# Kernel tuning notes

Hardware: AMD Instinct MI355X
Metric: run time of the kernel (lower is better)

The kernel has to match this reference:

```python
import jax, jax.numpy as jnp
import numpy as np

V = 100000   # vertices
C = 64       # in channels
D = 64       # out channels
W = 8        # weight matrices
DEG = 16     # neighbors per vertex
E = V * DEG  # edges


def setup_inputs() -> dict:
    key = jax.random.key(0)
    k = jax.random.split(key, 6)
    data = jax.random.normal(k[0], (V, C), dtype=jnp.float32)
    # fixed-degree adjacency: vertex i has DEG neighbors (arbitrary dst)
    edge_src = jnp.repeat(jnp.arange(V, dtype=jnp.int32), DEG)        # [E] sorted
    edge_dst = jax.random.randint(k[1], (E,), 0, V, dtype=jnp.int32)  # [E]
    edge_vals = jnp.full((E,), 1.0 / DEG, dtype=jnp.float32)          # row-normalized
    var_u = 0.1 * jax.random.normal(k[2], (C, W), dtype=jnp.float32)
    var_c = 0.1 * jax.random.normal(k[3], (W,), dtype=jnp.float32)
    var_w = 0.1 * jax.random.normal(k[4], (W, C, D), dtype=jnp.float32)
    var_b = 0.1 * jax.random.normal(k[5], (D,), dtype=jnp.float32)
    return {"data": data, "edge_src": edge_src, "edge_dst": edge_dst,
            "edge_vals": edge_vals, "var_u": var_u, "var_c": var_c,
            "var_w": var_w, "var_b": var_b}


def reference(data, edge_src, edge_dst, edge_vals, var_u, var_c, var_w, var_b):
    # translation_invariant=True => var_v = -var_u
    num_v = data.shape[0]
    x_u = data @ var_u            # [V, W]
    x_v = data @ (-var_u)         # [V, W]
    # edge logits and exp-normalize over the W weight matrices (softmax == exp/sum)
    logits = x_u[edge_src] + x_v[edge_dst] + var_c   # [E, W]
    q = jax.nn.softmax(logits, axis=-1)              # [E, W]
    # gathered neighbor features, pre-scaled by adjacency values
    x_sep = data[edge_dst] * edge_vals[:, None]      # [E, C]
    y = jnp.zeros((num_v, var_w.shape[-1]), dtype=data.dtype)
    for m in range(var_c.shape[0]):  # small fixed loop over W weight matrices
        agg = jax.ops.segment_sum(q[:, m:m + 1] * x_sep, edge_src,
                                  num_segments=num_v)  # [V, C]
        y = y + agg @ var_w[m]                          # [V, D]
    return y + var_b
```

## Files before the change

### kernel.cpp

```cpp
#include <hip/hip_runtime.h>

typedef _Float16 half2_t __attribute__((ext_vector_type(2)));
typedef _Float16 half4_t __attribute__((ext_vector_type(4)));
typedef _Float16 half8_t __attribute__((ext_vector_type(8)));
typedef __attribute__((ext_vector_type(4))) float f32x4;

#define NV 100000
#define NTILE 6250
#define GRID 512
#define LDSZ 81920

#define VMWAIT(N) asm volatile("s_waitcnt vmcnt(" #N ")" ::: "memory")
#define LGKM0     asm volatile("s_waitcnt lgkmcnt(0)" ::: "memory")
#define FENCE     asm volatile("" ::: "memory")

__device__ __forceinline__ unsigned cvt_pk_u(float a, float b) {
  auto h = __builtin_amdgcn_cvt_pkrtz(a, b);
  return __builtin_bit_cast(unsigned, h);
}
__device__ __forceinline__ half2_t u2h(unsigned u) { return __builtin_bit_cast(half2_t, u); }
__device__ __forceinline__ unsigned lds_off(const void* p) {
  return (unsigned)(size_t)(const __attribute__((address_space(3))) char*)p;
}
__device__ __forceinline__ void load16_to_lds(const void* g, void* s) {
  __builtin_amdgcn_global_load_lds(
      (const __attribute__((address_space(1))) unsigned int*)g,
      (__attribute__((address_space(3))) unsigned int*)s, 16, 0, 0);
}

__global__ __launch_bounds__(256) void k1_prep(const float* __restrict__ data,
                                               const float* __restrict__ var_u,
                                               const float* __restrict__ var_w,
                                               unsigned short* __restrict__ data_h,
                                               unsigned short* __restrict__ xu_h,
                                               unsigned short* __restrict__ Bt) {
  __shared__ float u_lds[512];
  int tid = threadIdx.x;
  if (blockIdx.x < 128) {
    int t = blockIdx.x * 256 + tid;
    int d = t >> 9, k = t & 511;
    _Float16 h = (_Float16)var_w[k * 64 + d];
    Bt[t] = __builtin_bit_cast(unsigned short, h);
  }
  u_lds[tid] = var_u[tid];
  u_lds[tid + 256] = var_u[tid + 256];
  __syncthreads();
  int v = blockIdx.x * 256 + tid;
  if (v >= NV) return;
  const float4* dp = (const float4*)(data + v * 64);
  float acc[8];
#pragma unroll
  for (int w = 0; w < 8; ++w) acc[w] = 0.f;
  uint4* ob = (uint4*)(data_h + v * 64);
#pragma unroll
  for (int q = 0; q < 8; ++q) {
    float4 a4 = dp[q * 2], b4 = dp[q * 2 + 1];
    int c0 = q * 8;
#pragma unroll
    for (int w = 0; w < 8; ++w)
      acc[w] += a4.x * u_lds[(c0 + 0) * 8 + w] + a4.y * u_lds[(c0 + 1) * 8 + w]
              + a4.z * u_lds[(c0 + 2) * 8 + w] + a4.w * u_lds[(c0 + 3) * 8 + w]
              + b4.x * u_lds[(c0 + 4) * 8 + w] + b4.y * u_lds[(c0 + 5) * 8 + w]
              + b4.z * u_lds[(c0 + 6) * 8 + w] + b4.w * u_lds[(c0 + 7) * 8 + w];
    uint4 pk;
    pk.x = cvt_pk_u(a4.x, a4.y); pk.y = cvt_pk_u(a4.z, a4.w);
    pk.z = cvt_pk_u(b4.x, b4.y); pk.w = cvt_pk_u(b4.z, b4.w);
    ob[q] = pk;
  }
  uint4 xp;
  xp.x = cvt_pk_u(acc[0], acc[1]); xp.y = cvt_pk_u(acc[2], acc[3]);
  xp.z = cvt_pk_u(acc[4], acc[5]); xp.w = cvt_pk_u(acc[6], acc[7]);
  *(uint4*)(xu_h + v * 8) = xp;
}

__global__ __launch_bounds__(256, 2) void k2_main(
    const unsigned short* __restrict__ data_h,
    const unsigned short* __restrict__ xu_h,
    const int* __restrict__ edge_dst,
    const float* __restrict__ edge_vals,
    const unsigned short* __restrict__ Bt,
    const float* __restrict__ var_c,
    const float* __restrict__ var_b,
    float* __restrict__ y) {
  extern __shared__ __align__(16) char smem[];
  char* XB0  = smem;
  char* XUD0 = smem + 65536;
  char* LIN0 = smem + 73728;

  int tid = threadIdx.x;
  int wave = tid >> 6;
  int l = tid & 63;
  int q4 = l >> 4;
  int row = l & 15;
  int col = row + wave * 16;

  uint4 btf[16];
#pragma unroll
  for (int ks = 0; ks < 16; ++ks)
    btf[ks] = *(const uint4*)(Bt + (col * 512 + ks * 32 + q4 * 8));
  float c8[8];
#pragma unroll
  for (int m = 0; m < 8; ++m) c8[m] = var_c[m];
  float bias = var_b[col];

#define LIN_DMA(SL, TS)                                                        \
  { char* lb_ = LIN0 + (SL) * 2048;                                            \
    if ((wave & 1) == 0)                                                       \
      load16_to_lds(edge_dst + (size_t)(TS) * 256 + l * 4, lb_);               \
    else                                                                       \
      load16_to_lds(edge_vals + (size_t)(TS) * 256 + l * 4, lb_ + 1024); }
#define XUD_DMA(SL, LSL)                                                       \
  { const int* ld_ = (const int*)(LIN0 + (LSL) * 2048);                        \
    int dv_ = ld_[wave * 64 + l];                                              \
    load16_to_lds(xu_h + (size_t)dv_ * 8, XUD0 + (SL) * 4096 + wave * 1024); }
#define X_DMA(SL, LSL)                                                         \
  { const int* ld_ = (const int*)(LIN0 + (LSL) * 2048);                        \
    int j_ = ((l >> 3) & 3) * 4 + ((l >> 1) & 3);                              \
    int ch0_ = ((l >> 5) << 1) | (l & 1);                                      \
    _Pragma("unroll")                                                          \
    for (int s_ = 0; s_ < 8; ++s_) {                                           \
      int dv_ = ld_[wave * 64 + (s_ >> 1) * 16 + j_];                          \
      int ch_ = ch0_ + (s_ & 1) * 4;                                           \
      load16_to_lds(data_h + (size_t)dv_ * 64 + ch_ * 8,                       \
                    XB0 + (SL) * 32768 + wave * 8192 + s_ * 1024); } }

  int t0 = blockIdx.x;
  int tG1 = (t0 + GRID < NTILE) ? t0 + GRID : t0;
  int tG2 = (t0 + 2 * GRID < NTILE) ? t0 + 2 * GRID : t0;
  FENCE;
  LIN_DMA(0, t0);
  LIN_DMA(1, tG1);
  LIN_DMA(2, tG2);
  FENCE;
  uint4 xsA = *(const uint4*)(xu_h + ((size_t)t0 * 16 + wave * 4 + q4) * 8);
  uint4 xsB = *(const uint4*)(xu_h + ((size_t)tG1 * 16 + wave * 4 + q4) * 8);
  VMWAIT(0);
  __builtin_amdgcn_s_barrier();
  FENCE;
  XUD_DMA(0, 0);
  X_DMA(0, 0);
  FENCE;
  VMWAIT(0);
  __builtin_amdgcn_s_barrier();

  int kc = 0;
  for (int t = t0; t < NTILE; t += GRID, ++kc) {
    int slc = kc & 1, lslc = kc & 3;
    int sl1 = (kc + 1) & 1, lsl1 = (kc + 1) & 3, lsl3 = (kc + 3) & 3;
    int t2c = (t + 2 * GRID < NTILE) ? t + 2 * GRID : t;
    int t3c = (t + 3 * GRID < NTILE) ? t + 3 * GRID : t;
    char* XBt = XB0 + slc * 32768;
    char* XUDt = XUD0 + slc * 4096;
    const char* LINt = LIN0 + lslc * 2048;

    FENCE;
    XUD_DMA(sl1, lsl1);
    X_DMA(sl1, lsl1);
    FENCE;

    {
      uint4 xd4 = *(const uint4*)(XUDt + (wave * 64 + l) * 16);
      float evv = ((const float*)(LINt + 1024))[wave * 64 + l];
      half2_t xm01 = u2h(xsA.x), xm23 = u2h(xsA.y), xm45 = u2h(xsA.z), xm67 = u2h(xsA.w);
      half2_t xd01 = u2h(xd4.x), xd23 = u2h(xd4.y), xd45 = u2h(xd4.z), xd67 = u2h(xd4.w);
      float ex0 = __expf((float)xm01[0] - (float)xd01[0] + c8[0]);
      float ex1 = __expf((float)xm01[1] - (float)xd01[1] + c8[1]);
      float ex2 = __expf((float)xm23[0] - (float)xd23[0] + c8[2]);
      float ex3 = __expf((float)xm23[1] - (float)xd23[1] + c8[3]);
      float ex4 = __expf((float)xm45[0] - (float)xd45[0] + c8[4]);
      float ex5 = __expf((float)xm45[1] - (float)xd45[1] + c8[5]);
      float ex6 = __expf((float)xm67[0] - (float)xd67[0] + c8[6]);
      float ex7 = __expf((float)xm67[1] - (float)xd67[1] + c8[7]);
      float ssum = ((ex0 + ex1) + (ex2 + ex3)) + ((ex4 + ex5) + (ex6 + ex7));
      float rs = __builtin_amdgcn_rcpf(ssum) * evv;
      uint4 qq;
      qq.x = cvt_pk_u(ex0 * rs, ex1 * rs);
      qq.y = cvt_pk_u(ex2 * rs, ex3 * rs);
      qq.z = cvt_pk_u(ex4 * rs, ex5 * rs);
      qq.w = cvt_pk_u(ex6 * rs, ex7 * rs);
      int vv = l >> 4, jq = (l >> 2) & 3, jl = l & 3;
      char* qb = XUDt + wave * 1024 + vv * 256;
#pragma unroll
      for (int m = 0; m < 8; ++m) {
        unsigned short hv = (unsigned short)((&qq.x)[m >> 1] >> ((m & 1) * 16));
        int byte = (((m ^ vv) & 7) << 5) + (((jq ^ vv ^ m) & 3) << 3) + jl * 2;
        *(unsigned short*)(qb + byte) = hv;
      }
    }

    uint4 xsC = *(const uint4*)(xu_h + ((size_t)t2c * 16 + wave * 4 + q4) * 8);
    FENCE;
    LIN_DMA(lsl3, t3c);
    FENCE;

    {
      uint2 qfr[4];
#pragma unroll
      for (int vv = 0; vv < 4; ++vv) {
        int srow = (row ^ vv) & 7;
        int gsl = (q4 ^ vv ^ row) & 3;
        qfr[vv] = *(const uint2*)(XUDt + wave * 1024 + vv * 256 + srow * 32 + gsl * 8);
      }
      unsigned xbase = lds_off(XBt + wave * 8192) + l * 8;
      uint2 trd[16];
#pragma unroll
      for (int vv = 0; vv < 4; ++vv)
#pragma unroll
        for (int cb = 0; cb < 4; ++cb) {
          unsigned a_ = xbase + vv * 2048 + cb * 512;
          asm volatile("ds_read_b64_tr_b16 %0, %1"
                       : "=v"(trd[vv * 4 + cb]) : "v"(a_) : "memory");
        }
      LGKM0;
      __builtin_amdgcn_sched_barrier(0);
      f32x4 D[16];
      __builtin_amdgcn_s_setprio(1);
#pragma unroll
      for (int vv = 0; vv < 4; ++vv)
#pragma unroll
        for (int cb = 0; cb < 4; ++cb) {
          f32x4 z = {0.f, 0.f, 0.f, 0.f};
          D[vv * 4 + cb] = __builtin_amdgcn_mfma_f32_16x16x16f16(
              __builtin_bit_cast(half4_t, trd[vv * 4 + cb]),
              __builtin_bit_cast(half4_t, qfr[vv]), z, 0, 0, 0);
        }
      __builtin_amdgcn_s_setprio(0);
      if (row < 8) {
#pragma unroll
        for (int vv = 0; vv < 4; ++vv) {
          int vg = wave * 4 + vv;
          char* ab = XBt + vg * 2048;
#pragma unroll
          for (int cb = 0; cb < 4; ++cb) {
            f32x4 d4 = D[vv * 4 + cb];
            uint2 w2;
            w2.x = cvt_pk_u(d4[0], d4[1]);
            w2.y = cvt_pk_u(d4[2], d4[3]);
            int byte = (row * 128 + cb * 32 + q4 * 8) ^ ((vg & 7) << 4)
                       ^ ((row & 3) << 5);
            *(uint2*)(ab + byte) = w2;
          }
        }
      }
    }
    LGKM0;
    __builtin_amdgcn_s_barrier();

    {
      f32x4 C0 = {0.f, 0.f, 0.f, 0.f};
      f32x4 C1 = {0.f, 0.f, 0.f, 0.f};
      __builtin_amdgcn_s_setprio(1);
#pragma unroll
      for (int ks2 = 0; ks2 < 8; ++ks2) {
        int ka = 2 * ks2, kb = 2 * ks2 + 1;
        int boa = (ka * 64 + q4 * 16) ^ ((row & 7) << 4) ^ (((ka >> 1) & 3) << 5);
        int bob = (kb * 64 + q4 * 16) ^ ((row & 7) << 4) ^ (((kb >> 1) & 3) << 5);
        half8_t afa = *(const half8_t*)(XBt + row * 2048 + boa);
        half8_t afb = *(const half8_t*)(XBt + row * 2048 + bob);
        C0 = __builtin_amdgcn_mfma_f32_16x16x32_f16(
            afa, __builtin_bit_cast(half8_t, btf[ka]), C0, 0, 0, 0);
        C1 = __builtin_amdgcn_mfma_f32_16x16x32_f16(
            afb, __builtin_bit_cast(half8_t, btf[kb]), C1, 0, 0, 0);
      }
      __builtin_amdgcn_s_setprio(0);
#pragma unroll
      for (int i = 0; i < 4; ++i)
        y[(size_t)(t * 16 + q4 * 4 + i) * 64 + col] = C0[i] + C1[i] + bias;
    }
    LGKM0;
    VMWAIT(4);
    __builtin_amdgcn_s_barrier();

    xsA = xsB; xsB = xsC;
  }
  VMWAIT(0);
#undef LIN_DMA
#undef XUD_DMA
#undef X_DMA
}

extern "C" void kernel_launch(void* const* d_in, const int* in_sizes, int n_in,
                              void* d_out, int out_size, void* d_ws, size_t ws_size,
                              hipStream_t stream) {
  const float* data      = (const float*)d_in[0];
  const int*   edge_dst  = (const int*)d_in[2];
  const float* edge_vals = (const float*)d_in[3];
  const float* var_u     = (const float*)d_in[4];
  const float* var_c     = (const float*)d_in[5];
  const float* var_w     = (const float*)d_in[6];
  const float* var_b     = (const float*)d_in[7];
  float* y = (float*)d_out;

  char* ws = (char*)d_ws;
  unsigned short* data_h = (unsigned short*)ws;
  unsigned short* xu_h   = (unsigned short*)(ws + 12800000);
  unsigned short* Bt     = (unsigned short*)(ws + 14400000);

  hipFuncSetAttribute((const void*)k2_main,
                      hipFuncAttributeMaxDynamicSharedMemorySize, LDSZ);

  hipLaunchKernelGGL(k1_prep, dim3((NV + 255) / 256), dim3(256), 0, stream,
                     data, var_u, var_w, data_h, xu_h, Bt);
  hipLaunchKernelGGL(k2_main, dim3(GRID), dim3(256), LDSZ, stream,
                     data_h, xu_h, edge_dst, edge_vals, Bt, var_c, var_b, y);
}
```

Baseline: 71.04 us.

## Software-pipeline softmax prepass one tile ahead of the aggregation stage

Moves the per-edge softmax/q computation for the next tile into the current iteration, after the transpose-read aggregation, waiting on only part of the outstanding DMA (vmcnt 8) for the next tile's XUD/LIN data. A prologue prepass handles the first tile. This removes the prepass from the head of each iteration so the exp work can overlap the in-flight loads and the previous stage's LDS traffic. It adds a partial vmcnt dependency that must match the DMA issue order, and it raises register pressure under the 2-waves launch bound.

```diff
diff --git a/kernel.cpp b/kernel.cpp
--- a/kernel.cpp
+++ b/kernel.cpp
@@ -73,6 +73,39 @@
   *(uint4*)(xu_h + v * 8) = xp;
 }
 
+#define PREPASS(XUDs, LINs, XS)                                               \
+  {                                                                           \
+    uint4 xd4 = *(const uint4*)((XUDs) + (wave * 64 + l) * 16);               \
+    float evv = ((const float*)((LINs) + 1024))[wave * 64 + l];               \
+    half2_t xm01 = u2h((XS).x), xm23 = u2h((XS).y);                           \
+    half2_t xm45 = u2h((XS).z), xm67 = u2h((XS).w);                           \
+    half2_t xd01 = u2h(xd4.x), xd23 = u2h(xd4.y);                             \
+    half2_t xd45 = u2h(xd4.z), xd67 = u2h(xd4.w);                             \
+    float ex0 = __expf((float)xm01[0] - (float)xd01[0] + c8[0]);              \
+    float ex1 = __expf((float)xm01[1] - (float)xd01[1] + c8[1]);              \
+    float ex2 = __expf((float)xm23[0] - (float)xd23[0] + c8[2]);              \
+    float ex3 = __expf((float)xm23[1] - (float)xd23[1] + c8[3]);              \
+    float ex4 = __expf((float)xm45[0] - (float)xd45[0] + c8[4]);              \
+    float ex5 = __expf((float)xm45[1] - (float)xd45[1] + c8[5]);              \
+    float ex6 = __expf((float)xm67[0] - (float)xd67[0] + c8[6]);              \
+    float ex7 = __expf((float)xm67[1] - (float)xd67[1] + c8[7]);              \
+    float ssum = ((ex0 + ex1) + (ex2 + ex3)) + ((ex4 + ex5) + (ex6 + ex7));   \
+    float rs = __builtin_amdgcn_rcpf(ssum) * evv;                             \
+    uint4 qq;                                                                 \
+    qq.x = cvt_pk_u(ex0 * rs, ex1 * rs);                                      \
+    qq.y = cvt_pk_u(ex2 * rs, ex3 * rs);                                      \
+    qq.z = cvt_pk_u(ex4 * rs, ex5 * rs);                                      \
+    qq.w = cvt_pk_u(ex6 * rs, ex7 * rs);                                      \
+    int vv = l >> 4, jq = (l >> 2) & 3, jl = l & 3;                           \
+    char* qb = (XUDs) + wave * 1024 + vv * 256;                               \
+    _Pragma("unroll")                                                         \
+    for (int m = 0; m < 8; ++m) {                                             \
+      unsigned short hv = (unsigned short)((&qq.x)[m >> 1] >> ((m & 1) * 16));\
+      int byte = (((m ^ vv) & 7) << 5) + (((jq ^ vv ^ m) & 3) << 3) + jl * 2; \
+      *(unsigned short*)(qb + byte) = hv;                                     \
+    }                                                                         \
+  }
+
 __global__ __launch_bounds__(256, 2) void k2_main(
     const unsigned short* __restrict__ data_h,
     const unsigned short* __restrict__ xu_h,
@@ -142,6 +175,8 @@
   FENCE;
   VMWAIT(0);
   __builtin_amdgcn_s_barrier();
+  PREPASS(XUD0, LIN0, xsA);
+  LGKM0;
 
   int kc = 0;
   for (int t = t0; t < NTILE; t += GRID, ++kc) {
@@ -151,46 +186,13 @@
     int t3c = (t + 3 * GRID < NTILE) ? t + 3 * GRID : t;
     char* XBt = XB0 + slc * 32768;
     char* XUDt = XUD0 + slc * 4096;
-    const char* LINt = LIN0 + lslc * 2048;
+    char* XUDn = XUD0 + sl1 * 4096;
+    const char* LINn = LIN0 + lsl1 * 2048;
+    (void)lslc;
 
     FENCE;
     XUD_DMA(sl1, lsl1);
     X_DMA(sl1, lsl1);
-    FENCE;
-
-    {
-      uint4 xd4 = *(const uint4*)(XUDt + (wave * 64 + l) * 16);
-      float evv = ((const float*)(LINt + 1024))[wave * 64 + l];
-      half2_t xm01 = u2h(xsA.x), xm23 = u2h(xsA.y), xm45 = u2h(xsA.z), xm67 = u2h(xsA.w);
-      half2_t xd01 = u2h(xd4.x), xd23 = u2h(xd4.y), xd45 = u2h(xd4.z), xd67 = u2h(xd4.w);
-      float ex0 = __expf((float)xm01[0] - (float)xd01[0] + c8[0]);
-      float ex1 = __expf((float)xm01[1] - (float)xd01[1] + c8[1]);
-      float ex2 = __expf((float)xm23[0] - (float)xd23[0] + c8[2]);
-      float ex3 = __expf((float)xm23[1] - (float)xd23[1] + c8[3]);
-      float ex4 = __expf((float)xm45[0] - (float)xd45[0] + c8[4]);
-      float ex5 = __expf((float)xm45[1] - (float)xd45[1] + c8[5]);
-      float ex6 = __expf((float)xm67[0] - (float)xd67[0] + c8[6]);
-      float ex7 = __expf((float)xm67[1] - (float)xd67[1] + c8[7]);
-      float ssum = ((ex0 + ex1) + (ex2 + ex3)) + ((ex4 + ex5) + (ex6 + ex7));
-      float rs = __builtin_amdgcn_rcpf(ssum) * evv;
-      uint4 qq;
-      qq.x = cvt_pk_u(ex0 * rs, ex1 * rs);
-      qq.y = cvt_pk_u(ex2 * rs, ex3 * rs);
-      qq.z = cvt_pk_u(ex4 * rs, ex5 * rs);
-      qq.w = cvt_pk_u(ex6 * rs, ex7 * rs);
-      int vv = l >> 4, jq = (l >> 2) & 3, jl = l & 3;
-      char* qb = XUDt + wave * 1024 + vv * 256;
-#pragma unroll
-      for (int m = 0; m < 8; ++m) {
-        unsigned short hv = (unsigned short)((&qq.x)[m >> 1] >> ((m & 1) * 16));
-        int byte = (((m ^ vv) & 7) << 5) + (((jq ^ vv ^ m) & 3) << 3) + jl * 2;
-        *(unsigned short*)(qb + byte) = hv;
-      }
-    }
-
-    uint4 xsC = *(const uint4*)(xu_h + ((size_t)t2c * 16 + wave * 4 + q4) * 8);
-    FENCE;
-    LIN_DMA(lsl3, t3c);
     FENCE;
 
     {
@@ -243,6 +245,16 @@
         }
       }
     }
+
+    VMWAIT(8);
+    PREPASS(XUDn, LINn, xsB);
+
+    FENCE;
+    uint4 xsC = *(const uint4*)(xu_h + ((size_t)t2c * 16 + wave * 4 + q4) * 8);
+    FENCE;
+    LIN_DMA(lsl3, t3c);
+    FENCE;
+
     LGKM0;
     __builtin_amdgcn_s_barrier();
 
@@ -271,7 +283,8 @@
     VMWAIT(4);
     __builtin_amdgcn_s_barrier();
 
-    xsA = xsB; xsB = xsC;
+    xsB = xsC;
+    (void)xsA;
   }
   VMWAIT(0);
 #undef LIN_DMA
```

Result: faster. 67.18 us (-5.4%).
